# Optimization experiments

Measured on AMD Instinct MI355X. Metric: run time of the kernel, lower is better.

The kernel has to match this reference:

```python
import jax, jax.numpy as jnp
import numpy as np
import math

B, T, D = 2, 2048, 2048
H, KV, Dh = 16, 4, 128
REP = H // KV
WINDOW = 1024
META = 128
ROPE_BASE = 10000.0


def _apply_rotary(x, pos):
    # x: (B, h, T, Dh), pos: (T,) -- interleaved (even/odd) RoPE as in the torch module
    dh = x.shape[-1]
    inv = 1.0 / (ROPE_BASE ** (jnp.arange(0, dh, 2, dtype=jnp.float32) / dh))  # (Dh/2,)
    freqs = pos.astype(jnp.float32)[:, None] * inv[None, :]                    # (T, Dh/2)
    cos = jnp.cos(freqs)[None, None].astype(x.dtype)
    sin = jnp.sin(freqs)[None, None].astype(x.dtype)
    x1, x2 = x[..., ::2], x[..., 1::2]
    o1 = x1 * cos - x2 * sin
    o2 = x1 * sin + x2 * cos
    return jnp.stack([o1, o2], axis=-1).reshape(x.shape)


def setup_inputs() -> dict:
    key = jax.random.key(0)
    ks = jax.random.split(key, 5)
    s = 0.02
    return {
        "x": jax.random.normal(ks[0], (B, T, D), jnp.float32),
        "Wq": jax.random.normal(ks[1], (D, H * Dh), jnp.float32) * s,
        "Wk": jax.random.normal(ks[2], (D, KV * Dh), jnp.float32) * s,
        "Wv": jax.random.normal(ks[3], (D, KV * Dh), jnp.float32) * s,
        "Wo": jax.random.normal(ks[4], (H * Dh, D), jnp.float32) * s,
    }


def reference(x, Wq, Wk, Wv, Wo):
    Bx, Tx, _ = x.shape
    # projections + head split: q (B,H,T,Dh); k,v (B,KV,T,Dh)
    q = (x @ Wq).reshape(Bx, Tx, H, Dh).transpose(0, 2, 1, 3)
    k = (x @ Wk).reshape(Bx, Tx, KV, Dh).transpose(0, 2, 1, 3)
    v = (x @ Wv).reshape(Bx, Tx, KV, Dh).transpose(0, 2, 1, 3)
    pos = jnp.arange(Tx)
    q = _apply_rotary(q, pos)
    k = _apply_rotary(k, pos)
    # GQA: repeat kv heads (expand+reshape == contiguous repeat along head axis)
    k_full = jnp.repeat(k, REP, axis=1)
    v_full = jnp.repeat(v, REP, axis=1)
    # sliding window: keep META meta tokens + last w content tokens
    w = min(WINDOW, Tx - META)
    k_full = jnp.concatenate([k_full[:, :, :META], k_full[:, :, Tx - w:]], axis=2)
    v_full = jnp.concatenate([v_full[:, :, :META], v_full[:, :, Tx - w:]], axis=2)
    Tk = META + w
    scores = jnp.einsum("bhqd,bhkd->bhqk", q, k_full) / math.sqrt(Dh)
    # torch: triu(full(-inf,(T,Tk)), diagonal=1) added to scores
    mask = jnp.arange(Tk)[None, :] > jnp.arange(Tx)[:, None]   # (T, Tk)
    scores = jnp.where(mask[None, None], -jnp.inf, scores)
    attn = jax.nn.softmax(scores, axis=-1)
    out = jnp.einsum("bhqk,bhkd->bhqd", attn, v_full)
    out = out.transpose(0, 2, 1, 3).reshape(Bx, Tx, H * Dh)
    return out @ Wo
```

## Files before the change

kernel.cpp:

```cpp
#include <hip/hip_runtime.h>
#include <hip/hip_bf16.h>
#include <math.h>

typedef __attribute__((ext_vector_type(4))) float f32x4;
typedef __attribute__((ext_vector_type(8))) short bf16x8;

#define LDSP(p)  ((__attribute__((address_space(3))) void*)(p))
#define GMEMP(p) ((const __attribute__((address_space(1))) void*)(p))

__device__ __forceinline__ short f2b(float f) {
  __hip_bfloat16 h = __float2bfloat16(f);
  return __builtin_bit_cast(short, h);
}
__device__ __forceinline__ float b2f(short s) {
  __hip_bfloat16 h = __builtin_bit_cast(__hip_bfloat16, s);
  return __bfloat162float(h);
}
__device__ __forceinline__ unsigned pack2(float a, float b) {
  return (unsigned)(unsigned short)f2b(a) | ((unsigned)(unsigned short)f2b(b) << 16);
}

__global__ void cvt_kernel(const float* __restrict__ src, short* __restrict__ dst, int n8) {
  int i = blockIdx.x * blockDim.x + threadIdx.x;
  if (i >= n8) return;
  const float4* s4 = (const float4*)src;
  float4 a = s4[2 * i], b = s4[2 * i + 1];
  bf16x8 o;
  o[0] = f2b(a.x); o[1] = f2b(a.y); o[2] = f2b(a.z); o[3] = f2b(a.w);
  o[4] = f2b(b.x); o[5] = f2b(b.y); o[6] = f2b(b.z); o[7] = f2b(b.w);
  *(bf16x8*)(dst + (size_t)i * 8) = o;
}

__global__ void transpose_all(const float* __restrict__ Wq, const float* __restrict__ Wk,
                              const float* __restrict__ Wv, const float* __restrict__ Wo,
                              short* __restrict__ wqkv_t, short* __restrict__ wo_t) {
  __shared__ float tile[32][33];
  int gx = blockIdx.x;
  const float* src; short* dst; int cols, cx;
  if (gx < 64)       { src = Wq; dst = wqkv_t;                        cols = 2048; cx = gx; }
  else if (gx < 80)  { src = Wk; dst = wqkv_t + (size_t)2048 * 2048;  cols = 512;  cx = gx - 64; }
  else if (gx < 96)  { src = Wv; dst = wqkv_t + (size_t)2560 * 2048;  cols = 512;  cx = gx - 80; }
  else               { src = Wo; dst = wo_t;                          cols = 2048; cx = gx - 96; }
  int c0 = cx * 32, r0 = blockIdx.y * 32;
  int tx = threadIdx.x & 31, ty = threadIdx.x >> 5;
  for (int i = ty; i < 32; i += 8)
    tile[i][tx] = src[(size_t)(r0 + i) * cols + c0 + tx];
  __syncthreads();
  for (int i = ty; i < 32; i += 8)
    dst[(size_t)(c0 + i) * 2048 + r0 + tx] = f2b(tile[tx][i]);
}

template <int OUTBF>
__global__ __launch_bounds__(256) void gemm_bt(const short* __restrict__ A,
                                               const short* __restrict__ Bt,
                                               void* __restrict__ Cv,
                                               int M, int N, int K) {
  __shared__ alignas(16) short As[3][128 * 32];
  __shared__ alignas(16) short Bs[3][128 * 32];
  const int m0 = blockIdx.y * 128, n0 = blockIdx.x * 128;
  const int wave = threadIdx.x >> 6, lane = threadIdx.x & 63;
  const int g = lane >> 4, cl = lane & 15;
  const int wr = (wave >> 1) * 64, wc = (wave & 1) * 64;
  const int tid = threadIdx.x;
  f32x4 acc[4][4];
#pragma unroll
  for (int i = 0; i < 4; ++i)
#pragma unroll
    for (int j = 0; j < 4; ++j) acc[i][j] = (f32x4){0.f, 0.f, 0.f, 0.f};

  const int e0 = tid * 8;
#define STAGE(kt, s)                                                                        \
  {                                                                                         \
    _Pragma("unroll") for (int c = 0; c < 2; ++c) {                                         \
      int e = c * 2048 + e0;                                                                \
      int r = e >> 5;                                                                       \
      int j = (e >> 3) & 3;                                                                 \
      int col = (kt) + 8 * (j ^ ((r >> 1) & 3));                                            \
      __builtin_amdgcn_global_load_lds(GMEMP(A + (size_t)(m0 + r) * K + col),               \
                                       LDSP(&As[s][e]), 16, 0, 0);                          \
      __builtin_amdgcn_global_load_lds(GMEMP(Bt + (size_t)(n0 + r) * K + col),              \
                                       LDSP(&Bs[s][e]), 16, 0, 0);                          \
    }                                                                                       \
  }

  const int nkt = K >> 5;
  STAGE(0, 0);
  STAGE(32, 1);
  asm volatile("s_waitcnt vmcnt(4)" ::: "memory");
  __builtin_amdgcn_s_barrier();
  asm volatile("" ::: "memory");

  int s = 0;
  for (int t = 0; t < nkt; ++t) {
    if (t + 2 < nkt) {
      int s2 = s + 2; if (s2 >= 3) s2 -= 3;
      STAGE((t + 2) << 5, s2);
    }
    bf16x8 af[4], bfr[4];
#pragma unroll
    for (int i = 0; i < 4; ++i) {
      int R = wr + 16 * i + cl;
      af[i] = *(const bf16x8*)&As[s][R * 32 + 8 * (g ^ ((R >> 1) & 3))];
    }
#pragma unroll
    for (int j = 0; j < 4; ++j) {
      int R = wc + 16 * j + cl;
      bfr[j] = *(const bf16x8*)&Bs[s][R * 32 + 8 * (g ^ ((R >> 1) & 3))];
    }
    __builtin_amdgcn_s_setprio(1);
#pragma unroll
    for (int i = 0; i < 4; ++i)
#pragma unroll
      for (int j = 0; j < 4; ++j)
        acc[i][j] = __builtin_amdgcn_mfma_f32_16x16x32_bf16(af[i], bfr[j], acc[i][j], 0, 0, 0);
    __builtin_amdgcn_s_setprio(0);
    asm volatile("s_waitcnt vmcnt(4)" ::: "memory");
    __builtin_amdgcn_s_barrier();
    asm volatile("" ::: "memory");
    if (++s >= 3) s -= 3;
  }
#undef STAGE
#pragma unroll
  for (int i = 0; i < 4; ++i)
#pragma unroll
    for (int j = 0; j < 4; ++j)
#pragma unroll
      for (int r = 0; r < 4; ++r) {
        int row = m0 + wr + 16 * i + 4 * g + r;
        int col = n0 + wc + 16 * j + cl;
        if (OUTBF)
          ((short*)Cv)[(size_t)row * N + col] = f2b(acc[i][j][r]);
        else
          ((float*)Cv)[(size_t)row * N + col] = acc[i][j][r];
      }
}

__global__ void pp_kernel(const short* __restrict__ qkv, short* __restrict__ qb,
                          short* __restrict__ ksel, short* __restrict__ vt) {
  int blk = blockIdx.x;
  if (blk < 16384) {
    int tid = blk * 256 + threadIdx.x;
    int i = tid & 63;
    int h = (tid >> 6) & 15;
    int row = tid >> 10;
    int t = row & 2047;
    int b = row >> 11;
    unsigned u = *(const unsigned*)(qkv + (size_t)row * 3072 + h * 128 + 2 * i);
    float x1 = b2f((short)(u & 0xffff));
    float x2 = b2f((short)(u >> 16));
    float inv = exp2f(-0.20762050593046f * (float)i);
    float ang = (float)t * inv;
    float sn, cs;
    __sincosf(ang, &sn, &cs);
    unsigned w = pack2(x1 * cs - x2 * sn, x1 * sn + x2 * cs);
    *(unsigned*)(qb + (size_t)((b * 16 + h) * 2048 + t) * 128 + 2 * i) = w;
  } else if (blk < 16384 + 4096) {
    int tid = (blk - 16384) * 256 + threadIdx.x;
    int i = tid & 63;
    int kvh = (tid >> 6) & 3;
    int row = tid >> 8;
    int t = row & 2047;
    int b = row >> 11;
    int idx = t < 128 ? t : (t >= 1024 ? t - 896 : -1);
    if (idx < 0) return;
    unsigned u = *(const unsigned*)(qkv + (size_t)row * 3072 + 2048 + kvh * 128 + 2 * i);
    float x1 = b2f((short)(u & 0xffff));
    float x2 = b2f((short)(u >> 16));
    float inv = exp2f(-0.20762050593046f * (float)i);
    float ang = (float)t * inv;
    float sn, cs;
    __sincosf(ang, &sn, &cs);
    unsigned w = pack2(x1 * cs - x2 * sn, x1 * sn + x2 * cs);
    *(unsigned*)(ksel + (size_t)((b * 4 + kvh) * 1152 + idx) * 128 + 2 * i) = w;
  } else {
    int tid = (blk - 20480) * 256 + threadIdx.x;
    int idx = tid % 1152;
    int rest = tid / 1152;
    int d = rest & 127;
    int kvh = (rest >> 7) & 3;
    int b = rest >> 9;
    int t = idx < 128 ? idx : idx + 896;
    vt[(size_t)((b * 4 + kvh) * 128 + d) * 1152 + idx] =
        qkv[(size_t)(b * 2048 + t) * 3072 + 2560 + kvh * 128 + d];
  }
}

__global__ __launch_bounds__(256) void attn_kernel(const short* __restrict__ qb,
                                                   const short* __restrict__ ksel,
                                                   const short* __restrict__ vt,
                                                   short* __restrict__ ao) {
  __shared__ alignas(16) short Ksm[2][8192];
  __shared__ alignas(16) short Vsm[2][8192];
  __shared__ alignas(16) short Psm[4][16][72];

  const int blk = blockIdx.x;
  const int qt = 31 - (blk >> 5);
  const int h = blk & 15, b = (blk >> 4) & 1;
  const int kv = h >> 2;
  const int wave = threadIdx.x >> 6, lane = threadIdx.x & 63;
  const int g = lane >> 4, cl = lane & 15;
  const int q0w = qt * 64 + wave * 16;
  const int qi = q0w + cl;
  const float scale = 0.08838834764831845f;
  const int niter = (qt + 1 < 18) ? (qt + 1) : 18;

  const short* kselb = ksel + (size_t)(b * 4 + kv) * 1152 * 128;
  const short* vtb = vt + (size_t)(b * 4 + kv) * 128 * 1152;

  const short* qrow = qb + (size_t)((b * 16 + h) * 2048 + qi) * 128;
  bf16x8 qf[4];
#pragma unroll
  for (int d = 0; d < 4; ++d) qf[d] = *(const bf16x8*)(qrow + d * 32 + 8 * g);

  f32x4 o[8];
#pragma unroll
  for (int c = 0; c < 8; ++c) o[c] = (f32x4){0.f, 0.f, 0.f, 0.f};
  float m_i = -1e30f, l_i = 0.f;

#define STAGEK(kk0, buf)                                                                  \
  {                                                                                       \
    _Pragma("unroll") for (int i = 0; i < 4; ++i) {                                       \
      int base = i * 2048 + wave * 512;                                                   \
      int Lel = base + lane * 8;                                                          \
      int kr = Lel >> 7;                                                                  \
      int kc = (Lel & 127) ^ ((kr & 7) << 3);                                             \
      __builtin_amdgcn_global_load_lds(GMEMP(kselb + (size_t)((kk0) + kr) * 128 + kc),    \
                                       LDSP(&Ksm[buf][base]), 16, 0, 0);                  \
    }                                                                                     \
  }
#define STAGEV(kk0, buf)                                                                  \
  {                                                                                       \
    _Pragma("unroll") for (int i = 0; i < 4; ++i) {                                       \
      int base = i * 2048 + wave * 512;                                                   \
      int Lel = base + lane * 8;                                                          \
      int vr = Lel >> 6;                                                                  \
      int vc = (Lel & 63) ^ ((vr & 7) << 3);                                              \
      __builtin_amdgcn_global_load_lds(GMEMP(vtb + (size_t)vr * 1152 + (kk0) + vc),       \
                                       LDSP(&Vsm[buf][base]), 16, 0, 0);                  \
    }                                                                                     \
  }

  STAGEK(0, 0);
  STAGEV(0, 0);
  asm volatile("s_waitcnt vmcnt(0)" ::: "memory");
  __builtin_amdgcn_s_barrier();
  asm volatile("" ::: "memory");

  for (int t = 0; t < niter; ++t) {
    const int cur = t & 1;
    const int kk0 = t * 64;
    if (t + 1 < niter) {
      STAGEK(kk0 + 64, cur ^ 1);
      STAGEV(kk0 + 64, cur ^ 1);
    }

    f32x4 sf[4];
#pragma unroll
    for (int j = 0; j < 4; ++j) sf[j] = (f32x4){0.f, 0.f, 0.f, 0.f};
    const short* kb = &Ksm[cur][0];
    const int sw = (cl & 7) << 3;
    __builtin_amdgcn_s_setprio(1);
#pragma unroll
    for (int j = 0; j < 4; ++j) {
      const int rs = (16 * j + cl) * 128;
#pragma unroll
      for (int d = 0; d < 4; ++d) {
        bf16x8 kf = *(const bf16x8*)&kb[rs + ((d * 32 + 8 * g) ^ sw)];
        sf[j] = __builtin_amdgcn_mfma_f32_16x16x32_bf16(kf, qf[d], sf[j], 0, 0, 0);
      }
    }
    __builtin_amdgcn_s_setprio(0);

    float sv[4][4];
    float mx = -1e30f;
#pragma unroll
    for (int j = 0; j < 4; ++j)
#pragma unroll
      for (int r = 0; r < 4; ++r) {
        int key = kk0 + 16 * j + 4 * g + r;
        float v = sf[j][r] * scale;
        v = (key <= qi) ? v : -1e30f;
        sv[j][r] = v;
        mx = fmaxf(mx, v);
      }
    mx = fmaxf(mx, __shfl_xor(mx, 16));
    mx = fmaxf(mx, __shfl_xor(mx, 32));
    const float mnew = fmaxf(m_i, mx);
    const float alpha = __expf(m_i - mnew);
    m_i = mnew;
    float ls = 0.f;
#pragma unroll
    for (int j = 0; j < 4; ++j) {
      float p0 = __expf(sv[j][0] - mnew);
      float p1 = __expf(sv[j][1] - mnew);
      float p2 = __expf(sv[j][2] - mnew);
      float p3 = __expf(sv[j][3] - mnew);
      ls += (p0 + p1) + (p2 + p3);
      uint2 w;
      w.x = pack2(p0, p1);
      w.y = pack2(p2, p3);
      *(uint2*)&Psm[wave][cl][16 * j + 4 * g] = w;
    }
    ls += __shfl_xor(ls, 16);
    ls += __shfl_xor(ls, 32);
    l_i = l_i * alpha + ls;
#pragma unroll
    for (int c = 0; c < 8; ++c)
#pragma unroll
      for (int r = 0; r < 4; ++r) o[c][r] *= alpha;

    asm volatile("s_waitcnt lgkmcnt(0)" ::: "memory");
    bf16x8 pb0 = *(const bf16x8*)&Psm[wave][cl][8 * g];
    bf16x8 pb1 = *(const bf16x8*)&Psm[wave][cl][32 + 8 * g];
    const short* vb = &Vsm[cur][0];
    __builtin_amdgcn_s_setprio(1);
#pragma unroll
    for (int c = 0; c < 8; ++c) {
      const int rvs = (c * 16 + cl) * 64;
      bf16x8 v0 = *(const bf16x8*)&vb[rvs + ((8 * g) ^ sw)];
      bf16x8 v1 = *(const bf16x8*)&vb[rvs + ((32 + 8 * g) ^ sw)];
      o[c] = __builtin_amdgcn_mfma_f32_16x16x32_bf16(v0, pb0, o[c], 0, 0, 0);
      o[c] = __builtin_amdgcn_mfma_f32_16x16x32_bf16(v1, pb1, o[c], 0, 0, 0);
    }
    __builtin_amdgcn_s_setprio(0);

    asm volatile("s_waitcnt vmcnt(0)" ::: "memory");
    __builtin_amdgcn_s_barrier();
    asm volatile("" ::: "memory");
  }
#undef STAGEK
#undef STAGEV

  short* Ol = &Ksm[0][0] + wave * 2176;
  const float invl = 1.0f / l_i;
#pragma unroll
  for (int c = 0; c < 8; ++c) {
    uint2 w;
    w.x = pack2(o[c][0] * invl, o[c][1] * invl);
    w.y = pack2(o[c][2] * invl, o[c][3] * invl);
    *(uint2*)&Ol[cl * 136 + c * 16 + 4 * g] = w;
  }
  asm volatile("s_waitcnt lgkmcnt(0)" ::: "memory");
  const int rowq = lane & 15, seg = lane >> 4;
  const short* srcl = Ol + rowq * 136 + seg * 32;
  short* dst = ao + (size_t)(b * 2048 + q0w + rowq) * 2048 + h * 128 + seg * 32;
#pragma unroll
  for (int k = 0; k < 4; ++k)
    *(bf16x8*)(dst + 8 * k) = *(const bf16x8*)(srcl + 8 * k);
}

extern "C" void kernel_launch(void* const* d_in, const int* in_sizes, int n_in,
                              void* d_out, int out_size, void* d_ws, size_t ws_size,
                              hipStream_t stream) {
  const float* x = (const float*)d_in[0];
  const float* Wq = (const float*)d_in[1];
  const float* Wk = (const float*)d_in[2];
  const float* Wv = (const float*)d_in[3];
  const float* Wo = (const float*)d_in[4];
  float* out = (float*)d_out;

  char* ws = (char*)d_ws;
  short* x_bf = (short*)ws;   ws += (size_t)4096 * 2048 * 2;
  short* wqkv_t = (short*)ws; ws += (size_t)3072 * 2048 * 2;
  short* wo_t = (short*)ws;   ws += (size_t)2048 * 2048 * 2;
  short* qkv = (short*)ws;    ws += (size_t)4096 * 3072 * 2;
  short* q_bf = (short*)ws;   ws += (size_t)2 * 16 * 2048 * 128 * 2;
  short* k_sel = (short*)ws;  ws += (size_t)2 * 4 * 1152 * 128 * 2;
  short* v_t = (short*)ws;    ws += (size_t)2 * 4 * 128 * 1152 * 2;
  short* ao = (short*)ws;     ws += (size_t)4096 * 2048 * 2;

  cvt_kernel<<<4096, 256, 0, stream>>>(x, x_bf, 1048576);
  transpose_all<<<dim3(160, 64), 256, 0, stream>>>(Wq, Wk, Wv, Wo, wqkv_t, wo_t);
  gemm_bt<1><<<dim3(24, 32), 256, 0, stream>>>(x_bf, wqkv_t, qkv, 4096, 3072, 2048);
  pp_kernel<<<25088, 256, 0, stream>>>(qkv, q_bf, k_sel, v_t);
  attn_kernel<<<1024, 256, 0, stream>>>(q_bf, k_sel, v_t, ao);
  gemm_bt<0><<<dim3(16, 32), 256, 0, stream>>>(ao, wo_t, out, 4096, 2048, 2048);
}
```

Baseline: 321.0 us.

## Fold softmax scale into Q, use exp2, skip masking and lazy rescale

Pre-multiplies Q by the attention scale and log2(e) during RoPE so the attention loop can use raw v_exp_f32 without a per-score multiply. The causal mask is now applied only on diagonal tiles. The running max and output rescale are updated only when some lane's new max exceeds the old by more than 8 in log2 units. The P tile is written with wider LDS stores in a different layout and read back in the matching order for the PV MFMA. This cuts VALU work in the softmax, at the cost of bf16 rounding of the scaled Q and bounded-growth exponentials under the lazy rescale.

```diff
diff --git a/kernel.cpp b/kernel.cpp
--- a/kernel.cpp
+++ b/kernel.cpp
@@ -18,6 +18,11 @@
 }
 __device__ __forceinline__ unsigned pack2(float a, float b) {
   return (unsigned)(unsigned short)f2b(a) | ((unsigned)(unsigned short)f2b(b) << 16);
+}
+__device__ __forceinline__ float exp2_fast(float x) {
+  float r;
+  asm("v_exp_f32 %0, %1" : "=v"(r) : "v"(x));
+  return r;
 }
 
 __global__ void cvt_kernel(const float* __restrict__ src, short* __restrict__ dst, int n8) {
@@ -139,6 +144,7 @@
                           short* __restrict__ ksel, short* __restrict__ vt) {
   int blk = blockIdx.x;
   if (blk < 16384) {
+    const float SCL = 0.08838834764831845f * 1.4426950408889634f;
     int tid = blk * 256 + threadIdx.x;
     int i = tid & 63;
     int h = (tid >> 6) & 15;
@@ -152,7 +158,7 @@
     float ang = (float)t * inv;
     float sn, cs;
     __sincosf(ang, &sn, &cs);
-    unsigned w = pack2(x1 * cs - x2 * sn, x1 * sn + x2 * cs);
+    unsigned w = pack2((x1 * cs - x2 * sn) * SCL, (x1 * sn + x2 * cs) * SCL);
     *(unsigned*)(qb + (size_t)((b * 16 + h) * 2048 + t) * 128 + 2 * i) = w;
   } else if (blk < 16384 + 4096) {
     int tid = (blk - 16384) * 256 + threadIdx.x;
@@ -201,8 +207,8 @@
   const int g = lane >> 4, cl = lane & 15;
   const int q0w = qt * 64 + wave * 16;
   const int qi = q0w + cl;
-  const float scale = 0.08838834764831845f;
   const int niter = (qt + 1 < 18) ? (qt + 1) : 18;
+  const int nfull = (qt < 18) ? qt : 18;
 
   const short* kselb = ksel + (size_t)(b * 4 + kv) * 1152 * 128;
   const short* vtb = vt + (size_t)(b * 4 + kv) * 128 * 1152;
@@ -271,47 +277,65 @@
     }
     __builtin_amdgcn_s_setprio(0);
 
-    float sv[4][4];
-    float mx = -1e30f;
-#pragma unroll
-    for (int j = 0; j < 4; ++j)
-#pragma unroll
-      for (int r = 0; r < 4; ++r) {
-        int key = kk0 + 16 * j + 4 * g + r;
-        float v = sf[j][r] * scale;
-        v = (key <= qi) ? v : -1e30f;
-        sv[j][r] = v;
-        mx = fmaxf(mx, v);
-      }
+    if (t >= nfull) {
+#pragma unroll
+      for (int j = 0; j < 4; ++j)
+#pragma unroll
+        for (int r = 0; r < 4; ++r) {
+          int key = kk0 + 16 * j + 4 * g + r;
+          sf[j][r] = (key <= qi) ? sf[j][r] : -3.0e38f;
+        }
+    }
+
+    float ma = fmaxf(fmaxf(fmaxf(sf[0][0], sf[0][1]), sf[0][2]), sf[0][3]);
+    float mb = fmaxf(fmaxf(fmaxf(sf[1][0], sf[1][1]), sf[1][2]), sf[1][3]);
+    float mc = fmaxf(fmaxf(fmaxf(sf[2][0], sf[2][1]), sf[2][2]), sf[2][3]);
+    float md = fmaxf(fmaxf(fmaxf(sf[3][0], sf[3][1]), sf[3][2]), sf[3][3]);
+    float mx = fmaxf(fmaxf(ma, mb), fmaxf(mc, md));
     mx = fmaxf(mx, __shfl_xor(mx, 16));
     mx = fmaxf(mx, __shfl_xor(mx, 32));
-    const float mnew = fmaxf(m_i, mx);
-    const float alpha = __expf(m_i - mnew);
-    m_i = mnew;
-    float ls = 0.f;
-#pragma unroll
-    for (int j = 0; j < 4; ++j) {
-      float p0 = __expf(sv[j][0] - mnew);
-      float p1 = __expf(sv[j][1] - mnew);
-      float p2 = __expf(sv[j][2] - mnew);
-      float p3 = __expf(sv[j][3] - mnew);
-      ls += (p0 + p1) + (p2 + p3);
-      uint2 w;
-      w.x = pack2(p0, p1);
-      w.y = pack2(p2, p3);
-      *(uint2*)&Psm[wave][cl][16 * j + 4 * g] = w;
-    }
+
+    if (!__all(mx <= m_i + 8.0f)) {
+      const float mnew = fmaxf(m_i, mx);
+      const float alpha = exp2_fast(m_i - mnew);
+      m_i = mnew;
+      l_i *= alpha;
+#pragma unroll
+      for (int c = 0; c < 8; ++c)
+#pragma unroll
+        for (int r = 0; r < 4; ++r) o[c][r] *= alpha;
+    }
+
+    float p[4][4];
+#pragma unroll
+    for (int j = 0; j < 4; ++j)
+#pragma unroll
+      for (int r = 0; r < 4; ++r) p[j][r] = exp2_fast(sf[j][r] - m_i);
+    float ls = ((p[0][0] + p[0][1]) + (p[0][2] + p[0][3])) +
+               ((p[1][0] + p[1][1]) + (p[1][2] + p[1][3])) +
+               ((p[2][0] + p[2][1]) + (p[2][2] + p[2][3])) +
+               ((p[3][0] + p[3][1]) + (p[3][2] + p[3][3]));
     ls += __shfl_xor(ls, 16);
     ls += __shfl_xor(ls, 32);
-    l_i = l_i * alpha + ls;
-#pragma unroll
-    for (int c = 0; c < 8; ++c)
-#pragma unroll
-      for (int r = 0; r < 4; ++r) o[c][r] *= alpha;
+    l_i += ls;
+    uint4 wA, wB;
+    wA.x = pack2(p[0][0], p[0][1]); wA.y = pack2(p[0][2], p[0][3]);
+    wA.z = pack2(p[1][0], p[1][1]); wA.w = pack2(p[1][2], p[1][3]);
+    wB.x = pack2(p[2][0], p[2][1]); wB.y = pack2(p[2][2], p[2][3]);
+    wB.z = pack2(p[3][0], p[3][1]); wB.w = pack2(p[3][2], p[3][3]);
+    *(uint4*)&Psm[wave][cl][16 * g] = wA;
+    *(uint4*)&Psm[wave][cl][16 * g + 8] = wB;
 
     asm volatile("s_waitcnt lgkmcnt(0)" ::: "memory");
-    bf16x8 pb0 = *(const bf16x8*)&Psm[wave][cl][8 * g];
-    bf16x8 pb1 = *(const bf16x8*)&Psm[wave][cl][32 + 8 * g];
+    const int S0 = 32 * (g & 1) + 4 * (g >> 1);
+    uint2 a0 = *(const uint2*)&Psm[wave][cl][S0];
+    uint2 a1 = *(const uint2*)&Psm[wave][cl][S0 + 16];
+    uint2 b0 = *(const uint2*)&Psm[wave][cl][S0 + 8];
+    uint2 b1 = *(const uint2*)&Psm[wave][cl][S0 + 24];
+    uint4 u0; u0.x = a0.x; u0.y = a0.y; u0.z = a1.x; u0.w = a1.y;
+    uint4 u1; u1.x = b0.x; u1.y = b0.y; u1.z = b1.x; u1.w = b1.y;
+    bf16x8 pb0 = __builtin_bit_cast(bf16x8, u0);
+    bf16x8 pb1 = __builtin_bit_cast(bf16x8, u1);
     const short* vb = &Vsm[cur][0];
     __builtin_amdgcn_s_setprio(1);
 #pragma unroll
```

Result: faster. 313.5 us (-2.3%).
